# Kernel optimization log

Hardware: AMD Instinct MI355X
Metric: run time of the kernel (lower is better)

## Reference

```python
import jax, jax.numpy as jnp
import numpy as np

H, HK, D, BLK, GH = 32, 8, 96, 64, 128   # q heads, kv heads, head_dim, gate block, gate hidden
HIDDEN = 3072
THR = 0.03
NEG = -1e30

def _rot_half(x):
    h = x.shape[-1] // 2
    return jnp.concatenate([-x[..., h:], x[..., :h]], axis=-1)

def setup_inputs() -> dict:
    key = jax.random.key(0)
    ks = jax.random.split(key, 6)
    B, S = 1, 2048
    hidden_states = jax.random.normal(ks[0], (B, S, HIDDEN), dtype=jnp.float32)
    # RoPE tables, theta = 10000
    inv_freq = 1.0 / (10000.0 ** (np.arange(0, D, 2, dtype=np.float32) / D))
    t = np.arange(S, dtype=np.float32)
    freqs = np.outer(t, inv_freq)                   # [S, D/2]
    emb = np.concatenate([freqs, freqs], axis=-1)   # [S, D]
    cos = jnp.asarray(np.cos(emb), dtype=jnp.float32)
    sin = jnp.asarray(np.sin(emb), dtype=jnp.float32)
    op = H * D + 2 * HK * D
    qkv_w = jax.random.normal(ks[1], (HIDDEN, op), dtype=jnp.float32) * 0.02
    o_w = jax.random.normal(ks[2], (H * D, HIDDEN), dtype=jnp.float32) * 0.02
    gate_wq = jax.random.normal(ks[3], (D, GH), dtype=jnp.float32) * 0.05
    gate_wk = jax.random.normal(ks[4], (2 * D, GH), dtype=jnp.float32) * 0.05
    return dict(hidden_states=hidden_states, cos=cos, sin=sin,
                qkv_w=qkv_w, o_w=o_w, gate_wq=gate_wq, gate_wk=gate_wk)

def reference(hidden_states, cos, sin, qkv_w, o_w, gate_wq, gate_wk):
    B, S, _ = hidden_states.shape
    G = H // HK            # GQA group size
    nB = S // BLK          # number of gate blocks
    scale = D ** -0.5

    # fused QKV projection and head split
    qkv = hidden_states @ qkv_w
    q = qkv[..., : H * D].reshape(B, S, H, D)
    k = qkv[..., H * D : H * D + HK * D].reshape(B, S, HK, D)
    v = qkv[..., H * D + HK * D :].reshape(B, S, HK, D)
    q_nope, k_nope = q, k

    # RoPE (unsqueeze over head dim)
    cs = cos[None, :, None, :]
    sn = sin[None, :, None, :]
    q = q * cs + _rot_half(q) * sn
    k = k * cs + _rot_half(k) * sn

    # ---- learned block-sparse gate (SeerAttention AttnGate) ----
    kb = k_nope.reshape(B, nB, BLK, HK, D)
    k_pool = jnp.concatenate([kb.mean(2), kb.max(2)], axis=-1)      # [B,nB,HK,2D] avg+max seq pooling
    k_gate = jnp.einsum('bnhe,eg->bnhg', k_pool, gate_wk)
    q_pool = q_nope.reshape(B, S, HK, G, D).mean(3)                 # q-head pooling to kv heads
    q_pool = q_pool.reshape(B, nB, BLK, HK, D).mean(2)              # block pooling
    q_gate = jnp.einsum('bnhd,dg->bnhg', q_pool, gate_wq)
    gate_logits = jnp.einsum('bqhg,bkhg->bhqk', q_gate, k_gate) * (GH ** -0.5)
    blk_causal = jnp.tril(jnp.ones((nB, nB), dtype=bool))
    gate_logits = jnp.where(blk_causal, gate_logits, NEG)
    gate_probs = jax.nn.softmax(gate_logits, axis=-1)
    block_mask = (gate_probs >= THR) & blk_causal                   # threshold sparsity method
    block_mask = block_mask | jnp.eye(nB, dtype=bool)               # diagonal block always active

    # expand block mask to token level, intersect with causal mask
    tok_mask = jnp.repeat(jnp.repeat(block_mask, BLK, axis=2), BLK, axis=3)  # [B,HK,S,S]
    causal = jnp.tril(jnp.ones((S, S), dtype=bool))
    mask = tok_mask & causal

    # ---- block-sparse masked attention with GQA ----
    qh = q.transpose(0, 2, 1, 3).reshape(B, HK, G, S, D)
    kh = k.transpose(0, 2, 1, 3)                                    # [B,HK,S,D]
    vh = v.transpose(0, 2, 1, 3)
    scores = jnp.einsum('bhgsd,bhtd->bhgst', qh, kh) * scale
    scores = jnp.where(mask[:, :, None], scores, NEG)
    attn = jax.nn.softmax(scores, axis=-1)
    out = jnp.einsum('bhgst,bhtd->bhgsd', attn, vh)                 # [B,HK,G,S,D]
    out = out.reshape(B, H, S, D).transpose(0, 2, 1, 3).reshape(B, S, H * D)
    return out @ o_w
```

## Files before the change

kernel.cpp:

```cpp
#include <hip/hip_runtime.h>
#include <hip/hip_bf16.h>
#include <math.h>

#define S_LEN 2048
#define HID 3072
#define NHEAD 32
#define NKV 8
#define HDIM 96
#define QKV_N 4608
#define NB 32
#define GHDIM 128

typedef __attribute__((ext_vector_type(8))) short bf16x8;
typedef __attribute__((ext_vector_type(4))) short bf16x4;
typedef __attribute__((ext_vector_type(4))) float f32x4;
typedef unsigned short ushort_t;

#define SCALE2 0.14724444754f

__device__ __forceinline__ unsigned short f2bf(float x) {
    unsigned u = __float_as_uint(x);
    u += 0x7fffu + ((u >> 16) & 1u);
    return (unsigned short)(u >> 16);
}
__device__ __forceinline__ unsigned packbf2(float a, float b) {
    return (unsigned)f2bf(a) | ((unsigned)f2bf(b) << 16);
}

#define GLOBAL_AS __attribute__((address_space(1)))
#define LDS_AS __attribute__((address_space(3)))
__device__ __forceinline__ void gl_lds16(const void* g, void* l) {
    __builtin_amdgcn_global_load_lds((const GLOBAL_AS unsigned int*)g,
                                     (LDS_AS unsigned int*)l, 16, 0, 0);
}
__device__ __forceinline__ void barrier_raw() {
    asm volatile("s_barrier" ::: "memory");
}

__global__ __launch_bounds__(256, 2) void gemm_bf16(const ushort_t* __restrict__ A,
                                                    const ushort_t* __restrict__ Bt,
                                                    float* __restrict__ C,
                                                    int M, int N, int K) {
    __shared__ ushort_t As[128 * 64];
    __shared__ ushort_t Bs[128 * 64];
    const int tid = threadIdx.x;
    const int lane = tid & 63;
    const int w = tid >> 6;
    const int wm = (w >> 1) * 64;
    const int wn = (w & 1) * 64;
    const int l15 = lane & 15;
    const int quad = lane >> 4;
    const int m0 = blockIdx.y * 128;
    const int n0 = blockIdx.x * 128;

    f32x4 acc[4][4] = {};

    for (int k0 = 0; k0 < K; k0 += 64) {
        __syncthreads();
#pragma unroll
        for (int j = 0; j < 4; ++j) {
            int s = j * 256 + w * 64 + lane;
            int row = s >> 3;
            int kc = (s & 7) ^ (row & 7);
            gl_lds16(A + (size_t)(m0 + row) * K + k0 + kc * 8,
                     &As[(j * 256 + w * 64) * 8]);
        }
#pragma unroll
        for (int j = 0; j < 4; ++j) {
            int s = j * 256 + w * 64 + lane;
            int row = s >> 3;
            int kc = (s & 7) ^ (row & 7);
            gl_lds16(Bt + (size_t)(n0 + row) * K + k0 + kc * 8,
                     &Bs[(j * 256 + w * 64) * 8]);
        }
        __syncthreads();
        bf16x8 af[2][4], bf[2][4];
#pragma unroll
        for (int mt = 0; mt < 4; ++mt) {
            int row = wm + mt * 16 + l15;
            int rx = row & 7;
#pragma unroll
            for (int ph = 0; ph < 2; ++ph)
                af[ph][mt] = *(const bf16x8*)&As[(row * 8 + ((ph * 4 + quad) ^ rx)) * 8];
        }
#pragma unroll
        for (int nt = 0; nt < 4; ++nt) {
            int row = wn + nt * 16 + l15;
            int rx = row & 7;
#pragma unroll
            for (int ph = 0; ph < 2; ++ph)
                bf[ph][nt] = *(const bf16x8*)&Bs[(row * 8 + ((ph * 4 + quad) ^ rx)) * 8];
        }
#pragma unroll
        for (int ph = 0; ph < 2; ++ph)
#pragma unroll
            for (int mt = 0; mt < 4; ++mt)
#pragma unroll
                for (int nt = 0; nt < 4; ++nt)
                    acc[mt][nt] = __builtin_amdgcn_mfma_f32_16x16x32_bf16(
                        af[ph][mt], bf[ph][nt], acc[mt][nt], 0, 0, 0);
    }
#pragma unroll
    for (int mt = 0; mt < 4; ++mt)
#pragma unroll
        for (int nt = 0; nt < 4; ++nt)
#pragma unroll
            for (int r = 0; r < 4; ++r) {
                int row = m0 + wm + mt * 16 + quad * 4 + r;
                int col = n0 + wn + nt * 16 + l15;
                C[(size_t)row * N + col] = acc[mt][nt][r];
            }
}

__global__ __launch_bounds__(256) void conv_bf16(const float* __restrict__ X,
                                                 ushort_t* __restrict__ Y, int n4) {
    int i = blockIdx.x * 256 + threadIdx.x;
    if (i >= n4) return;
    const float4 v = *(const float4*)(X + (size_t)i * 4);
    int2 p;
    p.x = (int)packbf2(v.x, v.y);
    p.y = (int)packbf2(v.z, v.w);
    *(int2*)(Y + (size_t)i * 4) = p;
}

__global__ __launch_bounds__(256) void transpose_convert(const float* __restrict__ W,
                                                         ushort_t* __restrict__ Wt,
                                                         int K, int N) {
    __shared__ float Ts[64][65];
    const int k0 = blockIdx.y * 64, n0 = blockIdx.x * 64;
    const int tid = threadIdx.x;
    {
        int r = tid >> 2, cq = tid & 3;
#pragma unroll
        for (int i = 0; i < 4; ++i) {
            int c = cq * 16 + i * 4;
            const float4 v = *(const float4*)(W + (size_t)(k0 + r) * N + n0 + c);
            Ts[r][c] = v.x; Ts[r][c + 1] = v.y; Ts[r][c + 2] = v.z; Ts[r][c + 3] = v.w;
        }
    }
    __syncthreads();
#pragma unroll
    for (int it = 0; it < 2; ++it) {
        int n = (tid >> 3) + it * 32;
        int kc = tid & 7;
        int4 r;
        r.x = (int)(packbf2(Ts[kc * 8 + 0][n], Ts[kc * 8 + 1][n]));
        r.y = (int)(packbf2(Ts[kc * 8 + 2][n], Ts[kc * 8 + 3][n]));
        r.z = (int)(packbf2(Ts[kc * 8 + 4][n], Ts[kc * 8 + 5][n]));
        r.w = (int)(packbf2(Ts[kc * 8 + 6][n], Ts[kc * 8 + 7][n]));
        *(int4*)(Wt + (size_t)(n0 + n) * K + k0 + kc * 8) = r;
    }
}

__global__ __launch_bounds__(128) void pool_gate_k_kernel(const float* __restrict__ qkv,
                                                          const float* __restrict__ gate_wk,
                                                          float* __restrict__ k_gate) {
    int nb = blockIdx.x, h = blockIdx.y;
    int tid = threadIdx.x;
    __shared__ float pool[192];
    if (tid < 96) {
        float s = 0.f, mx = -1e30f;
        for (int i = 0; i < 64; i++) {
            float v = qkv[(size_t)(nb * 64 + i) * QKV_N + HID + h * 96 + tid];
            s += v;
            mx = fmaxf(mx, v);
        }
        pool[tid] = s * (1.f / 64.f);
        pool[96 + tid] = mx;
    }
    __syncthreads();
    float acc = 0.f;
    for (int e = 0; e < 192; e++) acc += pool[e] * gate_wk[e * GHDIM + tid];
    k_gate[(size_t)(nb * NKV + h) * GHDIM + tid] = acc;
}

__global__ __launch_bounds__(128) void pool_gate_q_kernel(const float* __restrict__ qkv,
                                                          const float* __restrict__ gate_wq,
                                                          float* __restrict__ q_gate) {
    int nb = blockIdx.x, h = blockIdx.y;
    int tid = threadIdx.x;
    __shared__ float pool[96];
    if (tid < 96) {
        float s = 0.f;
        for (int i = 0; i < 64; i++)
            for (int g = 0; g < 4; g++)
                s += qkv[(size_t)(nb * 64 + i) * QKV_N + (h * 4 + g) * 96 + tid];
        pool[tid] = s * (1.f / 256.f);
    }
    __syncthreads();
    float acc = 0.f;
    for (int e = 0; e < 96; e++) acc += pool[e] * gate_wq[e * GHDIM + tid];
    q_gate[(size_t)(nb * NKV + h) * GHDIM + tid] = acc;
}

__global__ __launch_bounds__(64) void blockmask_kernel(const float* __restrict__ q_gate,
                                                       const float* __restrict__ k_gate,
                                                       int* __restrict__ mask) {
    int h = blockIdx.x, qb = blockIdx.y;
    int tid = threadIdx.x;
    __shared__ float logits[32];
    if (tid < 32) {
        if (tid <= qb) {
            float acc = 0.f;
            const float* qg = &q_gate[(size_t)(qb * NKV + h) * GHDIM];
            const float* kg = &k_gate[(size_t)(tid * NKV + h) * GHDIM];
            for (int e = 0; e < GHDIM; e++) acc += qg[e] * kg[e];
            logits[tid] = acc * 0.08838834764831845f;
        } else {
            logits[tid] = -1e30f;
        }
    }
    __syncthreads();
    if (tid < 32) {
        float mx = -1e30f;
        for (int j = 0; j <= qb; j++) mx = fmaxf(mx, logits[j]);
        float sum = 0.f;
        for (int j = 0; j <= qb; j++) sum += __expf(logits[j] - mx);
        float p = (tid <= qb) ? __expf(logits[tid] - mx) / sum : 0.f;
        int m = ((p >= 0.03f) && (tid <= qb)) || (tid == qb);
        mask[(h * NB + qb) * NB + tid] = m;
    }
}

__global__ __launch_bounds__(256) void rope_qk_kernel(const float* __restrict__ qkv,
                                                      const float* __restrict__ cosb,
                                                      const float* __restrict__ sinb,
                                                      ushort_t* __restrict__ Qb,
                                                      ushort_t* __restrict__ Kb) {
    int idx = blockIdx.x * 256 + threadIdx.x;
    int d = idx % 48;
    int tmp = idx / 48;
    int head = tmp % 40;
    int s = tmp / 40;
    float c0 = cosb[s * 96 + d], c1 = cosb[s * 96 + d + 48];
    float s0 = sinb[s * 96 + d], s1 = sinb[s * 96 + d + 48];
    if (head < 32) {
        size_t base = (size_t)s * QKV_N + head * 96;
        float x0 = qkv[base + d], x1 = qkv[base + d + 48];
        size_t ob = (size_t)s * HID + head * 96;
        Qb[ob + d] = f2bf((x0 * c0 - x1 * s0) * SCALE2);
        Qb[ob + d + 48] = f2bf((x1 * c1 + x0 * s1) * SCALE2);
    } else {
        int hh = head - 32;
        size_t base = (size_t)s * QKV_N + HID + hh * 96;
        float x0 = qkv[base + d], x1 = qkv[base + d + 48];
        size_t ob = ((size_t)hh * S_LEN + s) * 96;
        Kb[ob + d] = f2bf(x0 * c0 - x1 * s0);
        Kb[ob + d + 48] = f2bf(x1 * c1 + x0 * s1);
    }
}

__global__ __launch_bounds__(256) void transpose_v_kernel(const float* __restrict__ qkv,
                                                          ushort_t* __restrict__ Vtb) {
    __shared__ float Vs[64][97];
    const int ibk = blockIdx.x, h = blockIdx.y;
    const int tid = threadIdx.x;
    {
        int t = tid >> 2, cq = tid & 3;
#pragma unroll
        for (int i = 0; i < 6; ++i) {
            int c = cq * 24 + i * 4;
            const float4 v = *(const float4*)(qkv + (size_t)(ibk * 64 + t) * QKV_N +
                                              HID + 768 + h * 96 + c);
            Vs[t][c] = v.x; Vs[t][c + 1] = v.y; Vs[t][c + 2] = v.z; Vs[t][c + 3] = v.w;
        }
    }
    __syncthreads();
#pragma unroll
    for (int it = 0; it < 3; ++it) {
        int s = tid + it * 256;
        int d = s >> 3, tc = s & 7;
        int4 r;
        r.x = (int)(packbf2(Vs[tc * 8 + 0][d], Vs[tc * 8 + 1][d]));
        r.y = (int)(packbf2(Vs[tc * 8 + 2][d], Vs[tc * 8 + 3][d]));
        r.z = (int)(packbf2(Vs[tc * 8 + 4][d], Vs[tc * 8 + 5][d]));
        r.w = (int)(packbf2(Vs[tc * 8 + 6][d], Vs[tc * 8 + 7][d]));
        *(int4*)(Vtb + ((size_t)h * 96 + d) * S_LEN + ibk * 64 + tc * 8) = r;
    }
}

__global__ __launch_bounds__(256) void attn_mfma(const ushort_t* __restrict__ Qb,
                                                 const ushort_t* __restrict__ Kb,
                                                 const ushort_t* __restrict__ Vtb,
                                                 const int* __restrict__ mask,
                                                 ushort_t* __restrict__ out) {
    const int hq = blockIdx.x;
    const int ib = NB - 1 - (int)blockIdx.y;
    const int h = hq >> 2;
    const int tid = threadIdx.x;
    const int lane = tid & 63;
    const int w = tid >> 6;
    const int l15 = lane & 15;
    const int quad = lane >> 4;

    __shared__ ushort_t KsL[2][64 * 96];
    __shared__ ushort_t VtL[2][96 * 64];

    int pk[3];
    {
        int b0 = quad + (l15 & 7);
#pragma unroll
        for (int ks = 0; ks < 3; ++ks) {
            int p = b0 + ks * 4;
            if (p >= 12) p -= 12;
            if (p >= 12) p -= 12;
            pk[ks] = p;
        }
    }

    bf16x8 qf[3];
    {
        const ushort_t* qp = Qb + (size_t)(ib * 64 + w * 16 + l15) * HID + hq * 96;
#pragma unroll
        for (int ks = 0; ks < 3; ++ks)
            qf[ks] = *(const bf16x8*)(qp + ks * 32 + quad * 8);
    }

    const ushort_t* kbase = Kb + (size_t)h * S_LEN * 96;
    const ushort_t* vbase = Vtb + (size_t)h * 96 * S_LEN;

    unsigned long long bits =
        __ballot((lane <= ib) && (mask[(h * NB + ib) * NB + (lane & 31)] != 0));

    float m_i = -1e30f, l_i = 0.f;
    f32x4 acc_o[6] = {};

    auto stage = [&](int jb, int buf) {
#pragma unroll
        for (int j = 0; j < 3; ++j) {
            int s = j * 256 + w * 64 + lane;
            int t = (s * 2731) >> 15;
            int cpos = s - t * 12;
            int c = cpos - (t & 7);
            if (c < 0) c += 12;
            gl_lds16(kbase + (size_t)(jb * 64 + t) * 96 + c * 8,
                     &KsL[buf][(j * 256 + w * 64) * 8]);
        }
#pragma unroll
        for (int j = 0; j < 3; ++j) {
            int s = j * 256 + w * 64 + lane;
            int d = s >> 3;
            int tc = (s & 7) ^ (d & 7);
            gl_lds16(vbase + (size_t)d * S_LEN + jb * 64 + tc * 8,
                     &VtL[buf][(j * 256 + w * 64) * 8]);
        }
    };

    int jb = (int)__builtin_ctzll(bits);
    bits &= bits - 1;
    stage(jb, 0);
    int cur = 0;

    while (true) {
        int jn = -1;
        if (bits) {
            jn = (int)__builtin_ctzll(bits);
            bits &= bits - 1;
        }
        if (jn >= 0) {
            stage(jn, cur ^ 1);
            asm volatile("s_waitcnt vmcnt(6)" ::: "memory");
        } else {
            asm volatile("s_waitcnt vmcnt(0)" ::: "memory");
        }
        barrier_raw();

        const ushort_t* Kc = KsL[cur];
        const ushort_t* Vc = VtL[cur];

        f32x4 st[4] = {};
#pragma unroll
        for (int ks = 0; ks < 3; ++ks)
#pragma unroll
            for (int nt = 0; nt < 4; ++nt) {
                bf16x8 kb = *(const bf16x8*)&Kc[(nt * 16 + l15) * 96 + pk[ks] * 8];
                st[nt] = __builtin_amdgcn_mfma_f32_16x16x32_bf16(kb, qf[ks], st[nt], 0, 0, 0);
            }
        if (jb == ib) {
            int q = w * 16 + l15;
#pragma unroll
            for (int nt = 0; nt < 4; ++nt)
#pragma unroll
                for (int r = 0; r < 4; ++r)
                    if ((nt * 16 + quad * 4 + r) > q) st[nt][r] = -1e30f;
        }
        float mx = -1e30f;
#pragma unroll
        for (int nt = 0; nt < 4; ++nt)
#pragma unroll
            for (int r = 0; r < 4; ++r) mx = fmaxf(mx, st[nt][r]);
        mx = fmaxf(mx, __shfl_xor(mx, 16));
        mx = fmaxf(mx, __shfl_xor(mx, 32));
        float mnew = fmaxf(m_i, mx);
        float alpha = __builtin_amdgcn_exp2f(m_i - mnew);
        float ps = 0.f;
#pragma unroll
        for (int nt = 0; nt < 4; ++nt)
#pragma unroll
            for (int r = 0; r < 4; ++r) {
                float p = __builtin_amdgcn_exp2f(st[nt][r] - mnew);
                st[nt][r] = p;
                ps += p;
            }
        ps += __shfl_xor(ps, 16);
        ps += __shfl_xor(ps, 32);
        l_i = l_i * alpha + ps;
        m_i = mnew;
#pragma unroll
        for (int t = 0; t < 6; ++t)
#pragma unroll
            for (int r = 0; r < 4; ++r) acc_o[t][r] *= alpha;
        bf16x4 pf[4];
#pragma unroll
        for (int kblk = 0; kblk < 4; ++kblk) {
            union { bf16x4 v; unsigned u[2]; } pb;
            pb.u[0] = packbf2(st[kblk][0], st[kblk][1]);
            pb.u[1] = packbf2(st[kblk][2], st[kblk][3]);
            pf[kblk] = pb.v;
        }
#pragma unroll
        for (int kblk = 0; kblk < 4; ++kblk) {
            int cchunk = kblk * 2 + (quad >> 1);
            int eoff = (quad & 1) * 4;
#pragma unroll
            for (int dt = 0; dt < 6; ++dt) {
                int d = dt * 16 + l15;
                bf16x4 vf = *(const bf16x4*)&Vc[(d * 8 + (cchunk ^ (d & 7))) * 8 + eoff];
                acc_o[dt] = __builtin_amdgcn_mfma_f32_16x16x16bf16_1k(
                    vf, pf[kblk], acc_o[dt], 0, 0, 0);
            }
        }

        if (jn < 0) break;
        asm volatile("s_waitcnt lgkmcnt(0)" ::: "memory");
        barrier_raw();
        jb = jn;
        cur ^= 1;
    }

    float inv = 1.f / l_i;
    size_t orow = (size_t)(ib * 64 + w * 16 + l15) * HID + hq * 96;
#pragma unroll
    for (int dt = 0; dt < 6; ++dt) {
        int2 pkd;
        pkd.x = (int)packbf2(acc_o[dt][0] * inv, acc_o[dt][1] * inv);
        pkd.y = (int)packbf2(acc_o[dt][2] * inv, acc_o[dt][3] * inv);
        *(int2*)(out + orow + dt * 16 + quad * 4) = pkd;
    }
}

extern "C" void kernel_launch(void* const* d_in, const int* in_sizes, int n_in,
                              void* d_out, int out_size, void* d_ws, size_t ws_size,
                              hipStream_t stream) {
    const float* hidden  = (const float*)d_in[0];
    const float* cosb    = (const float*)d_in[1];
    const float* sinb    = (const float*)d_in[2];
    const float* qkv_w   = (const float*)d_in[3];
    const float* o_w     = (const float*)d_in[4];
    const float* gate_wq = (const float*)d_in[5];
    const float* gate_wk = (const float*)d_in[6];
    float* out = (float*)d_out;

    char* ws = (char*)d_ws;
    float*    qkv   = (float*)ws;
    ushort_t* h_bf  = (ushort_t*)(ws + 37748736);
    ushort_t* w1t   = (ushort_t*)(ws + 50331648);
    ushort_t* attn_out = (ushort_t*)(ws + 78643200);
    ushort_t* Kb    = (ushort_t*)(ws + 91226112);
    ushort_t* Vtb   = (ushort_t*)(ws + 95420416);
    float* k_gate   = (float*)(ws + 98566144);
    float* q_gate   = (float*)(ws + 98697216);
    int*   mask     = (int*)(ws + 98828288);
    ushort_t* Qb    = h_bf;
    ushort_t* o_wt  = (ushort_t*)qkv;

    conv_bf16<<<(S_LEN * HID / 4 + 255) / 256, 256, 0, stream>>>(hidden, h_bf, S_LEN * HID / 4);
    transpose_convert<<<dim3(QKV_N / 64, HID / 64), 256, 0, stream>>>(qkv_w, w1t, HID, QKV_N);
    gemm_bf16<<<dim3(QKV_N / 128, S_LEN / 128), 256, 0, stream>>>(h_bf, w1t, qkv, S_LEN, QKV_N, HID);
    pool_gate_k_kernel<<<dim3(NB, NKV), 128, 0, stream>>>(qkv, gate_wk, k_gate);
    pool_gate_q_kernel<<<dim3(NB, NKV), 128, 0, stream>>>(qkv, gate_wq, q_gate);
    blockmask_kernel<<<dim3(NKV, NB), 64, 0, stream>>>(q_gate, k_gate, mask);
    rope_qk_kernel<<<S_LEN * 40 * 48 / 256, 256, 0, stream>>>(qkv, cosb, sinb, Qb, Kb);
    transpose_v_kernel<<<dim3(NB, NKV), 256, 0, stream>>>(qkv, Vtb);
    transpose_convert<<<dim3(HID / 64, HID / 64), 256, 0, stream>>>(o_w, o_wt, HID, HID);
    attn_mfma<<<dim3(NHEAD, NB), 256, 0, stream>>>(Qb, Kb, Vtb, mask, attn_out);
    gemm_bf16<<<dim3(HID / 128, S_LEN / 128), 256, 0, stream>>>(attn_out, o_wt, out, S_LEN, HID, HID);
}
```

Baseline: 389.2 us.

## Store QKV GEMM output in bf16, fuse prep kernels, merge gate pooling kernels

The QKV GEMM now writes its output as bf16, plus a separate fp32 copy of only the K slice for the gate pooling. This halves the traffic that RoPE, V-transpose and Q pooling read afterwards. Input conversion and weight transpose are merged into one launch, RoPE, V-transpose and o_w transpose into another, and the two pooling kernels into one, which cuts launch count. GEMM launch bounds are raised to 4 blocks per CU. The risk is extra register pressure from the higher occupancy target, and Q/V now pass through bf16 before RoPE, which adds a little rounding.

```diff
diff --git a/kernel.cpp b/kernel.cpp
--- a/kernel.cpp
+++ b/kernel.cpp
@@ -10,6 +10,8 @@
 #define QKV_N 4608
 #define NB 32
 #define GHDIM 128
+#define KOFF 3072
+#define VOFF 3840
 
 typedef __attribute__((ext_vector_type(8))) short bf16x8;
 typedef __attribute__((ext_vector_type(4))) short bf16x4;
@@ -25,6 +27,9 @@
 }
 __device__ __forceinline__ unsigned packbf2(float a, float b) {
     return (unsigned)f2bf(a) | ((unsigned)f2bf(b) << 16);
+}
+__device__ __forceinline__ float bf2f(ushort_t u) {
+    return __uint_as_float(((unsigned)u) << 16);
 }
 
 #define GLOBAL_AS __attribute__((address_space(1)))
@@ -37,10 +42,12 @@
     asm volatile("s_barrier" ::: "memory");
 }
 
-__global__ __launch_bounds__(256, 2) void gemm_bf16(const ushort_t* __restrict__ A,
+__global__ __launch_bounds__(256, 4) void gemm_bf16(const ushort_t* __restrict__ A,
                                                     const ushort_t* __restrict__ Bt,
                                                     float* __restrict__ C,
-                                                    int M, int N, int K) {
+                                                    ushort_t* __restrict__ Cbf,
+                                                    float* __restrict__ CfK,
+                                                    int M, int N, int K, int mode) {
     __shared__ ushort_t As[128 * 64];
     __shared__ ushort_t Bs[128 * 64];
     const int tid = threadIdx.x;
@@ -100,22 +107,35 @@
                     acc[mt][nt] = __builtin_amdgcn_mfma_f32_16x16x32_bf16(
                         af[ph][mt], bf[ph][nt], acc[mt][nt], 0, 0, 0);
     }
-#pragma unroll
-    for (int mt = 0; mt < 4; ++mt)
-#pragma unroll
-        for (int nt = 0; nt < 4; ++nt)
-#pragma unroll
-            for (int r = 0; r < 4; ++r) {
-                int row = m0 + wm + mt * 16 + quad * 4 + r;
-                int col = n0 + wn + nt * 16 + l15;
-                C[(size_t)row * N + col] = acc[mt][nt][r];
-            }
-}
-
-__global__ __launch_bounds__(256) void conv_bf16(const float* __restrict__ X,
-                                                 ushort_t* __restrict__ Y, int n4) {
-    int i = blockIdx.x * 256 + threadIdx.x;
-    if (i >= n4) return;
+    if (mode == 0) {
+#pragma unroll
+        for (int mt = 0; mt < 4; ++mt)
+#pragma unroll
+            for (int nt = 0; nt < 4; ++nt)
+#pragma unroll
+                for (int r = 0; r < 4; ++r) {
+                    int row = m0 + wm + mt * 16 + quad * 4 + r;
+                    int col = n0 + wn + nt * 16 + l15;
+                    C[(size_t)row * N + col] = acc[mt][nt][r];
+                }
+    } else {
+        const bool isK = (n0 >= KOFF) && (n0 < VOFF);
+#pragma unroll
+        for (int mt = 0; mt < 4; ++mt)
+#pragma unroll
+            for (int nt = 0; nt < 4; ++nt)
+#pragma unroll
+                for (int r = 0; r < 4; ++r) {
+                    int row = m0 + wm + mt * 16 + quad * 4 + r;
+                    int col = n0 + wn + nt * 16 + l15;
+                    Cbf[(size_t)row * N + col] = f2bf(acc[mt][nt][r]);
+                    if (isK) CfK[(size_t)row * 768 + col - KOFF] = acc[mt][nt][r];
+                }
+    }
+}
+
+__device__ __forceinline__ void conv_body(const float* __restrict__ X,
+                                          ushort_t* __restrict__ Y, int i) {
     const float4 v = *(const float4*)(X + (size_t)i * 4);
     int2 p;
     p.x = (int)packbf2(v.x, v.y);
@@ -123,12 +143,10 @@
     *(int2*)(Y + (size_t)i * 4) = p;
 }
 
-__global__ __launch_bounds__(256) void transpose_convert(const float* __restrict__ W,
-                                                         ushort_t* __restrict__ Wt,
-                                                         int K, int N) {
+__device__ __forceinline__ void transpose_body(const float* __restrict__ W,
+                                               ushort_t* __restrict__ Wt,
+                                               int K, int N, int k0, int n0, int tid) {
     __shared__ float Ts[64][65];
-    const int k0 = blockIdx.y * 64, n0 = blockIdx.x * 64;
-    const int tid = threadIdx.x;
     {
         int r = tid >> 2, cq = tid & 3;
 #pragma unroll
@@ -152,45 +170,127 @@
     }
 }
 
-__global__ __launch_bounds__(128) void pool_gate_k_kernel(const float* __restrict__ qkv,
-                                                          const float* __restrict__ gate_wk,
-                                                          float* __restrict__ k_gate) {
+__global__ __launch_bounds__(256) void prep1(const float* __restrict__ hidden,
+                                             ushort_t* __restrict__ h_bf,
+                                             const float* __restrict__ qkv_w,
+                                             ushort_t* __restrict__ w1t) {
+    int id = blockIdx.x;
+    int tid = threadIdx.x;
+    if (id < 6144) {
+        conv_body(hidden, h_bf, id * 256 + tid);
+    } else {
+        int r = id - 6144;
+        transpose_body(qkv_w, w1t, HID, QKV_N, (r / 72) * 64, (r % 72) * 64, tid);
+    }
+}
+
+__global__ __launch_bounds__(256) void prep2(const ushort_t* __restrict__ qkv_bf,
+                                             const float* __restrict__ cosb,
+                                             const float* __restrict__ sinb,
+                                             ushort_t* __restrict__ Qb,
+                                             ushort_t* __restrict__ Kb,
+                                             ushort_t* __restrict__ Vtb,
+                                             const float* __restrict__ o_w,
+                                             ushort_t* __restrict__ o_wt) {
+    int id = blockIdx.x;
+    int tid = threadIdx.x;
+    if (id < 15360) {
+        int idx = id * 256 + tid;
+        int d = idx % 48;
+        int tmp = idx / 48;
+        int head = tmp % 40;
+        int s = tmp / 40;
+        float c0 = cosb[s * 96 + d], c1 = cosb[s * 96 + d + 48];
+        float s0 = sinb[s * 96 + d], s1 = sinb[s * 96 + d + 48];
+        if (head < 32) {
+            size_t base = (size_t)s * QKV_N + head * 96;
+            float x0 = bf2f(qkv_bf[base + d]), x1 = bf2f(qkv_bf[base + d + 48]);
+            size_t ob = (size_t)s * HID + head * 96;
+            Qb[ob + d] = f2bf((x0 * c0 - x1 * s0) * SCALE2);
+            Qb[ob + d + 48] = f2bf((x1 * c1 + x0 * s1) * SCALE2);
+        } else {
+            int hh = head - 32;
+            size_t base = (size_t)s * QKV_N + KOFF + hh * 96;
+            float x0 = bf2f(qkv_bf[base + d]), x1 = bf2f(qkv_bf[base + d + 48]);
+            size_t ob = ((size_t)hh * S_LEN + s) * 96;
+            Kb[ob + d] = f2bf(x0 * c0 - x1 * s0);
+            Kb[ob + d + 48] = f2bf(x1 * c1 + x0 * s1);
+        }
+    } else if (id < 15616) {
+        int r = id - 15360;
+        int ibk = r & 31, h = r >> 5;
+        __shared__ ushort_t Vs[64][104];
+        {
+            int rr = tid >> 2, seg = tid & 3;
+#pragma unroll
+            for (int j = 0; j < 3; ++j) {
+                int c = seg * 24 + j * 8;
+                const int4 v = *(const int4*)(qkv_bf + (size_t)(ibk * 64 + rr) * QKV_N +
+                                              VOFF + h * 96 + c);
+                *(int4*)&Vs[rr][c] = v;
+            }
+        }
+        __syncthreads();
+#pragma unroll
+        for (int it = 0; it < 3; ++it) {
+            int s = tid + it * 256;
+            int d = s >> 3, tc = s & 7;
+            int4 o;
+            o.x = (int)Vs[tc * 8 + 0][d] | ((int)Vs[tc * 8 + 1][d] << 16);
+            o.y = (int)Vs[tc * 8 + 2][d] | ((int)Vs[tc * 8 + 3][d] << 16);
+            o.z = (int)Vs[tc * 8 + 4][d] | ((int)Vs[tc * 8 + 5][d] << 16);
+            o.w = (int)Vs[tc * 8 + 6][d] | ((int)Vs[tc * 8 + 7][d] << 16);
+            *(int4*)(Vtb + ((size_t)h * 96 + d) * S_LEN + ibk * 64 + tc * 8) = o;
+        }
+    } else {
+        int r = id - 15616;
+        transpose_body(o_w, o_wt, HID, HID, (r / 48) * 64, (r % 48) * 64, tid);
+    }
+}
+
+__global__ __launch_bounds__(256) void pool_gate_kernel(const float* __restrict__ qkvK,
+                                                        const ushort_t* __restrict__ qkv_bf,
+                                                        const float* __restrict__ gate_wk,
+                                                        const float* __restrict__ gate_wq,
+                                                        float* __restrict__ k_gate,
+                                                        float* __restrict__ q_gate) {
     int nb = blockIdx.x, h = blockIdx.y;
     int tid = threadIdx.x;
-    __shared__ float pool[192];
-    if (tid < 96) {
-        float s = 0.f, mx = -1e30f;
-        for (int i = 0; i < 64; i++) {
-            float v = qkv[(size_t)(nb * 64 + i) * QKV_N + HID + h * 96 + tid];
-            s += v;
-            mx = fmaxf(mx, v);
-        }
-        pool[tid] = s * (1.f / 64.f);
-        pool[96 + tid] = mx;
+    __shared__ float poolk[192];
+    __shared__ float poolq[96];
+    if (tid < 128) {
+        if (tid < 96) {
+            float s = 0.f, mx = -1e30f;
+            for (int i = 0; i < 64; i++) {
+                float v = qkvK[(size_t)(nb * 64 + i) * 768 + h * 96 + tid];
+                s += v;
+                mx = fmaxf(mx, v);
+            }
+            poolk[tid] = s * (1.f / 64.f);
+            poolk[96 + tid] = mx;
+        }
+    } else {
+        int t2 = tid - 128;
+        if (t2 < 96) {
+            float s = 0.f;
+            for (int i = 0; i < 64; i++)
+#pragma unroll
+                for (int g = 0; g < 4; g++)
+                    s += bf2f(qkv_bf[(size_t)(nb * 64 + i) * QKV_N + (h * 4 + g) * 96 + t2]);
+            poolq[t2] = s * (1.f / 256.f);
+        }
     }
     __syncthreads();
-    float acc = 0.f;
-    for (int e = 0; e < 192; e++) acc += pool[e] * gate_wk[e * GHDIM + tid];
-    k_gate[(size_t)(nb * NKV + h) * GHDIM + tid] = acc;
-}
-
-__global__ __launch_bounds__(128) void pool_gate_q_kernel(const float* __restrict__ qkv,
-                                                          const float* __restrict__ gate_wq,
-                                                          float* __restrict__ q_gate) {
-    int nb = blockIdx.x, h = blockIdx.y;
-    int tid = threadIdx.x;
-    __shared__ float pool[96];
-    if (tid < 96) {
-        float s = 0.f;
-        for (int i = 0; i < 64; i++)
-            for (int g = 0; g < 4; g++)
-                s += qkv[(size_t)(nb * 64 + i) * QKV_N + (h * 4 + g) * 96 + tid];
-        pool[tid] = s * (1.f / 256.f);
-    }
-    __syncthreads();
-    float acc = 0.f;
-    for (int e = 0; e < 96; e++) acc += pool[e] * gate_wq[e * GHDIM + tid];
-    q_gate[(size_t)(nb * NKV + h) * GHDIM + tid] = acc;
+    if (tid < 128) {
+        float acc = 0.f;
+        for (int e = 0; e < 192; e++) acc += poolk[e] * gate_wk[e * GHDIM + tid];
+        k_gate[(size_t)(nb * NKV + h) * GHDIM + tid] = acc;
+    } else {
+        int t2 = tid - 128;
+        float acc = 0.f;
+        for (int e = 0; e < 96; e++) acc += poolq[e] * gate_wq[e * GHDIM + t2];
+        q_gate[(size_t)(nb * NKV + h) * GHDIM + t2] = acc;
+    }
 }
 
 __global__ __launch_bounds__(64) void blockmask_kernel(const float* __restrict__ q_gate,
@@ -222,63 +322,6 @@
     }
 }
 
-__global__ __launch_bounds__(256) void rope_qk_kernel(const float* __restrict__ qkv,
-                                                      const float* __restrict__ cosb,
-                                                      const float* __restrict__ sinb,
-                                                      ushort_t* __restrict__ Qb,
-                                                      ushort_t* __restrict__ Kb) {
-    int idx = blockIdx.x * 256 + threadIdx.x;
-    int d = idx % 48;
-    int tmp = idx / 48;
-    int head = tmp % 40;
-    int s = tmp / 40;
-    float c0 = cosb[s * 96 + d], c1 = cosb[s * 96 + d + 48];
-    float s0 = sinb[s * 96 + d], s1 = sinb[s * 96 + d + 48];
-    if (head < 32) {
-        size_t base = (size_t)s * QKV_N + head * 96;
-        float x0 = qkv[base + d], x1 = qkv[base + d + 48];
-        size_t ob = (size_t)s * HID + head * 96;
-        Qb[ob + d] = f2bf((x0 * c0 - x1 * s0) * SCALE2);
-        Qb[ob + d + 48] = f2bf((x1 * c1 + x0 * s1) * SCALE2);
-    } else {
-        int hh = head - 32;
-        size_t base = (size_t)s * QKV_N + HID + hh * 96;
-        float x0 = qkv[base + d], x1 = qkv[base + d + 48];
-        size_t ob = ((size_t)hh * S_LEN + s) * 96;
-        Kb[ob + d] = f2bf(x0 * c0 - x1 * s0);
-        Kb[ob + d + 48] = f2bf(x1 * c1 + x0 * s1);
-    }
-}
-
-__global__ __launch_bounds__(256) void transpose_v_kernel(const float* __restrict__ qkv,
-                                                          ushort_t* __restrict__ Vtb) {
-    __shared__ float Vs[64][97];
-    const int ibk = blockIdx.x, h = blockIdx.y;
-    const int tid = threadIdx.x;
-    {
-        int t = tid >> 2, cq = tid & 3;
-#pragma unroll
-        for (int i = 0; i < 6; ++i) {
-            int c = cq * 24 + i * 4;
-            const float4 v = *(const float4*)(qkv + (size_t)(ibk * 64 + t) * QKV_N +
-                                              HID + 768 + h * 96 + c);
-            Vs[t][c] = v.x; Vs[t][c + 1] = v.y; Vs[t][c + 2] = v.z; Vs[t][c + 3] = v.w;
-        }
-    }
-    __syncthreads();
-#pragma unroll
-    for (int it = 0; it < 3; ++it) {
-        int s = tid + it * 256;
-        int d = s >> 3, tc = s & 7;
-        int4 r;
-        r.x = (int)(packbf2(Vs[tc * 8 + 0][d], Vs[tc * 8 + 1][d]));
-        r.y = (int)(packbf2(Vs[tc * 8 + 2][d], Vs[tc * 8 + 3][d]));
-        r.z = (int)(packbf2(Vs[tc * 8 + 4][d], Vs[tc * 8 + 5][d]));
-        r.w = (int)(packbf2(Vs[tc * 8 + 6][d], Vs[tc * 8 + 7][d]));
-        *(int4*)(Vtb + ((size_t)h * 96 + d) * S_LEN + ibk * 64 + tc * 8) = r;
-    }
-}
-
 __global__ __launch_bounds__(256) void attn_mfma(const ushort_t* __restrict__ Qb,
                                                  const ushort_t* __restrict__ Kb,
                                                  const ushort_t* __restrict__ Vtb,
@@ -462,27 +505,27 @@
     float* out = (float*)d_out;
 
     char* ws = (char*)d_ws;
-    float*    qkv   = (float*)ws;
-    ushort_t* h_bf  = (ushort_t*)(ws + 37748736);
-    ushort_t* w1t   = (ushort_t*)(ws + 50331648);
-    ushort_t* attn_out = (ushort_t*)(ws + 78643200);
-    ushort_t* Kb    = (ushort_t*)(ws + 91226112);
-    ushort_t* Vtb   = (ushort_t*)(ws + 95420416);
-    float* k_gate   = (float*)(ws + 98566144);
-    float* q_gate   = (float*)(ws + 98697216);
-    int*   mask     = (int*)(ws + 98828288);
-    ushort_t* Qb    = h_bf;
-    ushort_t* o_wt  = (ushort_t*)qkv;
-
-    conv_bf16<<<(S_LEN * HID / 4 + 255) / 256, 256, 0, stream>>>(hidden, h_bf, S_LEN * HID / 4);
-    transpose_convert<<<dim3(QKV_N / 64, HID / 64), 256, 0, stream>>>(qkv_w, w1t, HID, QKV_N);
-    gemm_bf16<<<dim3(QKV_N / 128, S_LEN / 128), 256, 0, stream>>>(h_bf, w1t, qkv, S_LEN, QKV_N, HID);
-    pool_gate_k_kernel<<<dim3(NB, NKV), 128, 0, stream>>>(qkv, gate_wk, k_gate);
-    pool_gate_q_kernel<<<dim3(NB, NKV), 128, 0, stream>>>(qkv, gate_wq, q_gate);
+    ushort_t* qkv_bf   = (ushort_t*)ws;
+    float*    qkv_f32K = (float*)(ws + 18874368);
+    ushort_t* h_bf     = (ushort_t*)(ws + 25165824);
+    ushort_t* w1t      = (ushort_t*)(ws + 37748736);
+    ushort_t* attn_out = (ushort_t*)(ws + 66060288);
+    ushort_t* Kb       = (ushort_t*)(ws + 78643200);
+    ushort_t* Vtb      = (ushort_t*)(ws + 81788928);
+    float*    k_gate   = (float*)(ws + 84934656);
+    float*    q_gate   = (float*)(ws + 85065728);
+    int*      mask     = (int*)(ws + 85196800);
+    ushort_t* Qb   = h_bf;
+    ushort_t* o_wt = w1t;
+
+    prep1<<<9600, 256, 0, stream>>>(hidden, h_bf, qkv_w, w1t);
+    gemm_bf16<<<dim3(QKV_N / 128, S_LEN / 128), 256, 0, stream>>>(
+        h_bf, w1t, nullptr, qkv_bf, qkv_f32K, S_LEN, QKV_N, HID, 1);
+    pool_gate_kernel<<<dim3(NB, NKV), 256, 0, stream>>>(qkv_f32K, qkv_bf,
+                                                        gate_wk, gate_wq, k_gate, q_gate);
     blockmask_kernel<<<dim3(NKV, NB), 64, 0, stream>>>(q_gate, k_gate, mask);
-    rope_qk_kernel<<<S_LEN * 40 * 48 / 256, 256, 0, stream>>>(qkv, cosb, sinb, Qb, Kb);
-    transpose_v_kernel<<<dim3(NB, NKV), 256, 0, stream>>>(qkv, Vtb);
-    transpose_convert<<<dim3(HID / 64, HID / 64), 256, 0, stream>>>(o_w, o_wt, HID, HID);
+    prep2<<<17920, 256, 0, stream>>>(qkv_bf, cosb, sinb, Qb, Kb, Vtb, o_w, o_wt);
     attn_mfma<<<dim3(NHEAD, NB), 256, 0, stream>>>(Qb, Kb, Vtb, mask, attn_out);
-    gemm_bf16<<<dim3(HID / 128, S_LEN / 128), 256, 0, stream>>>(attn_out, o_wt, out, S_LEN, HID, HID);
-}
+    gemm_bf16<<<dim3(HID / 128, S_LEN / 128), 256, 0, stream>>>(
+        attn_out, o_wt, out, nullptr, nullptr, S_LEN, HID, HID, 0);
+}
```

Measured after the change: 382.0 us. About the same (-1.8%).
